# Performance work log

Measured on AMD Instinct MI355X. Metric: run time of the kernel, lower is better.

## Reference

```python
import jax, jax.numpy as jnp
import numpy as np

D_MODEL = 768
NUM_HEADS = 6
SPARSITY = 0.1
HEAD_DIM = D_MODEL // NUM_HEADS
SCALE = HEAD_DIM ** -0.5
B, C = 8, 4096


def setup_inputs() -> dict:
    key = jax.random.key(0)
    k1, k2 = jax.random.split(key, 2)
    x = jax.random.normal(k1, (B, C, D_MODEL), dtype=jnp.float32)
    # to_qkv: Linear(d_model, 3*d_model); torch layout W:[out,in], b:[out]
    W = jax.random.normal(k2, (3 * D_MODEL, D_MODEL), dtype=jnp.float32) * (D_MODEL ** -0.5)
    b = jnp.zeros((3 * D_MODEL,), dtype=jnp.float32)
    return {"x": x, "W": W, "b": b}


def reference(x, W, b):
    Bb, Cc, X = x.shape
    H, Dh = NUM_HEADS, HEAD_DIM
    n = Bb * Cc
    qkv = (x.reshape(n, X) @ W.T + b).reshape(n, 3, H, Dh)
    q, k, v = qkv[:, 0], qkv[:, 1], qkv[:, 2]  # each [n, H, Dh]
    # per-token attention across heads: [n, H, H]
    scores = jnp.einsum('nhd,ngd->nhg', q, k) * SCALE
    k_heads = max(1, int(H * SPARSITY))
    topk_scores, topk_idx = jax.lax.top_k(scores, k_heads)  # [n, H, k]
    soft = jax.nn.softmax(topk_scores, axis=-1)
    # sparse_attn @ v == weighted gather of v rows at topk_idx (zeros elsewhere)
    v_g = jnp.take_along_axis(v[:, None, :, :], topk_idx[..., None], axis=2)  # [n, H, k, Dh]
    out = jnp.einsum('nhk,nhkd->nhd', soft, v_g)  # [n, H, Dh]
    # torch: out.transpose(1, 2).reshape(B, C, d_model)  (3D tensor -> swap H and Dh)
    out = jnp.swapaxes(out, 1, 2).reshape(Bb, Cc, X)
    channel_importance = jnp.linalg.norm(out, axis=-1)  # [B, C]
    k_channels = max(1, int(Cc * SPARSITY))
    _, ch_idx = jax.lax.top_k(channel_importance, k_channels)  # [B, k_channels]
    sparse_feat = jnp.take_along_axis(out, ch_idx[:, :, None], axis=1)  # [B, k_channels, d_model]
    return sparse_feat, ch_idx, k_channels
```

## Files before the change

### kernel.cpp

```cpp
#include <hip/hip_runtime.h>
#include <cstdint>
#include <cstddef>

#pragma clang fp contract(off)

#define NROWS 32768
#define NCOLS 2304
#define DMODEL 768
#define QK 1536
#define KCH 409
#define NBATCH 8
#define FEAT_ELEMS ((size_t)NBATCH * KCH * DMODEL)
#define SCALE_F 0.08838834764831845f

#define BM 128
#define BN 128
#define BK 32
#define RS 140

__device__ __forceinline__ int chunk_off(int c) { return 8 * c + 4 * (c >> 2); }

__global__ __launch_bounds__(256) void gemm_qkv_f32(
    const float* __restrict__ x, const float* __restrict__ W,
    const float* __restrict__ bias, float* __restrict__ qkv)
{
    __shared__ float As[BK * RS];
    __shared__ float Bs[BK * RS];

    const int tid = threadIdx.x;
    const int tx = tid & 15;
    const int ty = tid >> 4;
    const int n0 = blockIdx.x * BN;
    const int m0 = blockIdx.y * BM;

    const int sm  = tid >> 3;
    const int sk4 = (tid & 7) << 2;

    const float* xa = x + (size_t)(m0 + sm) * DMODEL + sk4;
    const float* wb = W + (size_t)(n0 + sm) * DMODEL + sk4;

    const int aoff = chunk_off(ty);
    const int boff = chunk_off(tx);
    const int wsub = sm & 7;
    const int wchk = sm >> 3;

    float4 pa[4], pb[4];
    #pragma unroll
    for (int i = 0; i < 4; ++i) {
        pa[i] = *(const float4*)(xa + (size_t)(32 * i) * DMODEL);
        pb[i] = *(const float4*)(wb + (size_t)(32 * i) * DMODEL);
    }

    float acc[8][8] = {};

    for (int kt = 0; kt < DMODEL / BK; ++kt) {
        __syncthreads();
        #pragma unroll
        for (int i = 0; i < 4; ++i) {
            const int co = chunk_off(wchk + 4 * i) + wsub;
            As[(sk4 + 0) * RS + co] = pa[i].x;
            As[(sk4 + 1) * RS + co] = pa[i].y;
            As[(sk4 + 2) * RS + co] = pa[i].z;
            As[(sk4 + 3) * RS + co] = pa[i].w;
            Bs[(sk4 + 0) * RS + co] = pb[i].x;
            Bs[(sk4 + 1) * RS + co] = pb[i].y;
            Bs[(sk4 + 2) * RS + co] = pb[i].z;
            Bs[(sk4 + 3) * RS + co] = pb[i].w;
        }
        __syncthreads();

        if (kt + 1 < DMODEL / BK) {
            const int ko = (kt + 1) * BK;
            #pragma unroll
            for (int i = 0; i < 4; ++i) {
                pa[i] = *(const float4*)(xa + (size_t)(32 * i) * DMODEL + ko);
                pb[i] = *(const float4*)(wb + (size_t)(32 * i) * DMODEL + ko);
            }
        }

        #pragma unroll 8
        for (int k = 0; k < BK; ++k) {
            const float* ar = &As[k * RS + aoff];
            const float* br = &Bs[k * RS + boff];
            const float4 a0 = *(const float4*)(ar);
            const float4 a1 = *(const float4*)(ar + 4);
            const float4 b0 = *(const float4*)(br);
            const float4 b1 = *(const float4*)(br + 4);
            const float a[8] = {a0.x, a0.y, a0.z, a0.w, a1.x, a1.y, a1.z, a1.w};
            const float b[8] = {b0.x, b0.y, b0.z, b0.w, b1.x, b1.y, b1.z, b1.w};
            #pragma unroll
            for (int i = 0; i < 8; ++i)
                #pragma unroll
                for (int j = 0; j < 8; ++j)
                    acc[i][j] = fmaf(a[i], b[j], acc[i][j]);
        }
    }

    const int col = n0 + 8 * tx;
    float bcol[8];
    #pragma unroll
    for (int j = 0; j < 8; ++j) bcol[j] = bias[col + j];

    #pragma unroll
    for (int i = 0; i < 8; ++i) {
        const int row = m0 + 8 * ty + i;
        float4 o0, o1;
        o0.x = acc[i][0] + bcol[0];
        o0.y = acc[i][1] + bcol[1];
        o0.z = acc[i][2] + bcol[2];
        o0.w = acc[i][3] + bcol[3];
        o1.x = acc[i][4] + bcol[4];
        o1.y = acc[i][5] + bcol[5];
        o1.z = acc[i][6] + bcol[6];
        o1.w = acc[i][7] + bcol[7];
        *(float4*)(&qkv[(size_t)row * NCOLS + col])     = o0;
        *(float4*)(&qkv[(size_t)row * NCOLS + col + 4]) = o1;
    }
}

__global__ __launch_bounds__(256) void select_and_norm(
    const float* __restrict__ qkv, float* __restrict__ norms,
    uint64_t* __restrict__ gstar)
{
    __shared__ float rowbuf[4][NCOLS];
    __shared__ float sc[4][36];
    __shared__ int   gs_s[4][6];
    __shared__ float sblk[4][8];

    const int tid  = threadIdx.x;
    const int wave = tid >> 6;
    const int lane = tid & 63;
    const int n = blockIdx.x * 4 + wave;

    {
        const float4* src = (const float4*)(qkv + (size_t)n * NCOLS);
        float4* dst = (float4*)(&rowbuf[wave][0]);
        #pragma unroll
        for (int i = 0; i < 9; ++i) dst[lane + 64 * i] = src[lane + 64 * i];
    }
    __syncthreads();

    if (lane < 36) {
        const int h = lane / 6, g = lane % 6;
        const float* qh = &rowbuf[wave][h * 128];
        const float* kh = &rowbuf[wave][768 + g * 128];
        float s = 0.0f;
        for (int d = 0; d < 128; ++d)
            s = s + qh[d] * kh[d];
        sc[wave][lane] = s * SCALE_F;
    }
    __syncthreads();

    if (lane < 6) {
        float best = sc[wave][lane * 6];
        int bg = 0;
        #pragma unroll
        for (int g = 1; g < 6; ++g) {
            const float v = sc[wave][lane * 6 + g];
            if (v > best) { best = v; bg = g; }
        }
        gs_s[wave][lane] = bg;
    }
    __syncthreads();

    if (lane < 8) {
        const float* vr = &rowbuf[wave][QK];
        int gtab[6];
        #pragma unroll
        for (int h = 0; h < 6; ++h) gtab[h] = gs_s[wave][h];

        float r8[8];
        #pragma unroll
        for (int jj = 0; jj < 8; ++jj) {
            const int f = 96 * lane + jj;
            const float v = vr[gtab[f % 6] * 128 + f / 6];
            r8[jj] = v * v;
        }
        for (int i = 8; i < 96; i += 8) {
            #pragma unroll
            for (int jj = 0; jj < 8; ++jj) {
                const int f = 96 * lane + i + jj;
                const float v = vr[gtab[f % 6] * 128 + f / 6];
                r8[jj] = r8[jj] + v * v;
            }
        }
        sblk[wave][lane] = ((r8[0] + r8[1]) + (r8[2] + r8[3]))
                         + ((r8[4] + r8[5]) + (r8[6] + r8[7]));
    }
    __syncthreads();

    if (lane == 0) {
        const float* s = sblk[wave];
        float n2 = ((s[0] + s[1]) + (s[2] + s[3]))
                 + ((s[4] + s[5]) + (s[6] + s[7]));
        norms[n] = sqrtf(n2);
        uint64_t pk = 0;
        #pragma unroll
        for (int h = 0; h < 6; ++h)
            pk |= (uint64_t)gs_s[wave][h] << (8 * h);
        gstar[n] = pk;
    }
}

__global__ __launch_bounds__(256) void topk_channels(
    const float* __restrict__ norms, int* __restrict__ chidx,
    float* __restrict__ out)
{
    __shared__ float vals[4096];
    __shared__ float rv[256];
    __shared__ int   ri[256];
    const int b = blockIdx.x, t = threadIdx.x;

    for (int i = t; i < 4096; i += 256)
        vals[i] = norms[(size_t)b * 4096 + i];
    __syncthreads();

    for (int j = 0; j < KCH; ++j) {
        float best = -1.0f;
        int bi = 0;
        #pragma unroll
        for (int u = 0; u < 16; ++u) {
            const int i = t + 256 * u;
            const float v = vals[i];
            if (v > best) { best = v; bi = i; }
        }
        rv[t] = best; ri[t] = bi;
        __syncthreads();
        for (int s2 = 128; s2 > 0; s2 >>= 1) {
            if (t < s2) {
                const float ov = rv[t + s2]; const int oi = ri[t + s2];
                if (ov > rv[t] || (ov == rv[t] && oi < ri[t])) { rv[t] = ov; ri[t] = oi; }
            }
            __syncthreads();
        }
        if (t == 0) {
            const int w = ri[0];
            chidx[b * KCH + j] = w;
            out[FEAT_ELEMS + (size_t)b * KCH + j] = (float)w;
            vals[w] = -1.0f;
        }
        __syncthreads();
    }
    if (b == 0 && t == 0)
        out[FEAT_ELEMS + (size_t)NBATCH * KCH] = (float)KCH;
}

__global__ __launch_bounds__(256) void gather_sparse(
    const float* __restrict__ qkv, const uint64_t* __restrict__ gstar,
    const int* __restrict__ chidx, float* __restrict__ out)
{
    const int bj = blockIdx.x;
    const int b = bj / KCH;
    const int ch = chidx[bj];
    const int n = b * 4096 + ch;
    const uint64_t pk = gstar[n];
    for (int f = threadIdx.x; f < DMODEL; f += 256) {
        const int h = f % 6;
        const int d = f / 6;
        const int g = (int)((pk >> (8 * h)) & 7u);
        out[(size_t)bj * DMODEL + f] = qkv[(size_t)n * NCOLS + QK + g * 128 + d];
    }
}

extern "C" void kernel_launch(void* const* d_in, const int* in_sizes, int n_in,
                              void* d_out, int out_size, void* d_ws, size_t ws_size,
                              hipStream_t stream)
{
    const float* x    = (const float*)d_in[0];
    const float* W    = (const float*)d_in[1];
    const float* bias = (const float*)d_in[2];
    float* out = (float*)d_out;
    char*  ws  = (char*)d_ws;

    const size_t qkvBytes   = (size_t)NROWS * NCOLS * sizeof(float);
    const size_t normsBytes = (size_t)NROWS * sizeof(float);
    const size_t gstarBytes = (size_t)NROWS * sizeof(uint64_t);
    const size_t chidxBytes = (size_t)NBATCH * KCH * sizeof(int);
    const size_t baseBytes  = qkvBytes + normsBytes + gstarBytes + chidxBytes;
    if (ws_size < baseBytes) return;

    float*    qkv   = (float*)ws;
    float*    norms = (float*)(ws + qkvBytes);
    uint64_t* gstar = (uint64_t*)(ws + qkvBytes + normsBytes);
    int*      chidx = (int*)(ws + qkvBytes + normsBytes + gstarBytes);

    gemm_qkv_f32<<<dim3(NCOLS / BN, NROWS / BM), 256, 0, stream>>>(x, W, bias, qkv);
    select_and_norm<<<NROWS / 4, 256, 0, stream>>>(qkv, norms, gstar);
    topk_channels<<<NBATCH, 256, 0, stream>>>(norms, chidx, out);
    gather_sparse<<<NBATCH * KCH, 256, 0, stream>>>(qkv, gstar, chidx, out);
}
```

Measured before the change: 1.996 ms.

## Enlarge QKV GEMM tile to 256x128 with XOR-swizzled shared memory layout

Doubles the M tile of the fp32 QKV GEMM so each thread computes a 16x8 accumulator block, raising FMA work per shared-memory load. The shared-memory chunk placement is XOR-permuted by k-group to avoid bank conflicts, with separate row strides for the A and B tiles. Launch bounds now request two blocks per CU. The 128 accumulators plus prefetch registers raise register pressure and could cause spills or lower occupancy.

```diff
diff --git a/kernel.cpp b/kernel.cpp
--- a/kernel.cpp
+++ b/kernel.cpp
@@ -13,19 +13,20 @@
 #define FEAT_ELEMS ((size_t)NBATCH * KCH * DMODEL)
 #define SCALE_F 0.08838834764831845f
 
-#define BM 128
+#define BM 256
 #define BN 128
 #define BK 32
-#define RS 140
+#define RSA 284
+#define RSB 140
 
 __device__ __forceinline__ int chunk_off(int c) { return 8 * c + 4 * (c >> 2); }
 
-__global__ __launch_bounds__(256) void gemm_qkv_f32(
+__global__ __launch_bounds__(256, 2) void gemm_qkv_f32(
     const float* __restrict__ x, const float* __restrict__ W,
     const float* __restrict__ bias, float* __restrict__ qkv)
 {
-    __shared__ float As[BK * RS];
-    __shared__ float Bs[BK * RS];
+    __shared__ float As[BK * RSA];
+    __shared__ float Bs[BK * RSB];
 
     const int tid = threadIdx.x;
     const int tx = tid & 15;
@@ -35,64 +36,78 @@
 
     const int sm  = tid >> 3;
     const int sk4 = (tid & 7) << 2;
+    const int perm_s = (sk4 >> 2) & 7;
+    const int wsub = sm & 7;
+    const int wchk = sm >> 3;
 
     const float* xa = x + (size_t)(m0 + sm) * DMODEL + sk4;
     const float* wb = W + (size_t)(n0 + sm) * DMODEL + sk4;
 
-    const int aoff = chunk_off(ty);
-    const int boff = chunk_off(tx);
-    const int wsub = sm & 7;
-    const int wchk = sm >> 3;
-
-    float4 pa[4], pb[4];
-    #pragma unroll
-    for (int i = 0; i < 4; ++i) {
-        pa[i] = *(const float4*)(xa + (size_t)(32 * i) * DMODEL);
-        pb[i] = *(const float4*)(wb + (size_t)(32 * i) * DMODEL);
-    }
-
-    float acc[8][8] = {};
+    int coa[8], cob[4];
+    #pragma unroll
+    for (int i = 0; i < 8; ++i) coa[i] = chunk_off((wchk + 4 * i) ^ perm_s) + wsub;
+    #pragma unroll
+    for (int i = 0; i < 4; ++i) cob[i] = chunk_off((wchk + 4 * i) ^ perm_s) + wsub;
+
+    float4 pa[8], pb[4];
+    #pragma unroll
+    for (int i = 0; i < 8; ++i) pa[i] = *(const float4*)(xa + (size_t)(32 * i) * DMODEL);
+    #pragma unroll
+    for (int i = 0; i < 4; ++i) pb[i] = *(const float4*)(wb + (size_t)(32 * i) * DMODEL);
+
+    float acc[16][8] = {};
 
     for (int kt = 0; kt < DMODEL / BK; ++kt) {
         __syncthreads();
         #pragma unroll
+        for (int i = 0; i < 8; ++i) {
+            As[(sk4 + 0) * RSA + coa[i]] = pa[i].x;
+            As[(sk4 + 1) * RSA + coa[i]] = pa[i].y;
+            As[(sk4 + 2) * RSA + coa[i]] = pa[i].z;
+            As[(sk4 + 3) * RSA + coa[i]] = pa[i].w;
+        }
+        #pragma unroll
         for (int i = 0; i < 4; ++i) {
-            const int co = chunk_off(wchk + 4 * i) + wsub;
-            As[(sk4 + 0) * RS + co] = pa[i].x;
-            As[(sk4 + 1) * RS + co] = pa[i].y;
-            As[(sk4 + 2) * RS + co] = pa[i].z;
-            As[(sk4 + 3) * RS + co] = pa[i].w;
-            Bs[(sk4 + 0) * RS + co] = pb[i].x;
-            Bs[(sk4 + 1) * RS + co] = pb[i].y;
-            Bs[(sk4 + 2) * RS + co] = pb[i].z;
-            Bs[(sk4 + 3) * RS + co] = pb[i].w;
+            Bs[(sk4 + 0) * RSB + cob[i]] = pb[i].x;
+            Bs[(sk4 + 1) * RSB + cob[i]] = pb[i].y;
+            Bs[(sk4 + 2) * RSB + cob[i]] = pb[i].z;
+            Bs[(sk4 + 3) * RSB + cob[i]] = pb[i].w;
         }
         __syncthreads();
 
         if (kt + 1 < DMODEL / BK) {
             const int ko = (kt + 1) * BK;
             #pragma unroll
-            for (int i = 0; i < 4; ++i) {
+            for (int i = 0; i < 8; ++i)
                 pa[i] = *(const float4*)(xa + (size_t)(32 * i) * DMODEL + ko);
+            #pragma unroll
+            for (int i = 0; i < 4; ++i)
                 pb[i] = *(const float4*)(wb + (size_t)(32 * i) * DMODEL + ko);
+        }
+
+        #pragma unroll
+        for (int p = 0; p < 8; ++p) {
+            const float* Ap0 = &As[chunk_off((2 * ty) ^ p)];
+            const float* Ap1 = &As[chunk_off((2 * ty + 1) ^ p)];
+            const float* Bp  = &Bs[chunk_off(tx ^ p)];
+            #pragma unroll
+            for (int kq = 0; kq < 4; ++kq) {
+                const int k = 4 * p + kq;
+                const float4 a0 = *(const float4*)(Ap0 + k * RSA);
+                const float4 a1 = *(const float4*)(Ap0 + k * RSA + 4);
+                const float4 a2 = *(const float4*)(Ap1 + k * RSA);
+                const float4 a3 = *(const float4*)(Ap1 + k * RSA + 4);
+                const float4 b0 = *(const float4*)(Bp + k * RSB);
+                const float4 b1 = *(const float4*)(Bp + k * RSB + 4);
+                const float a[16] = {a0.x, a0.y, a0.z, a0.w, a1.x, a1.y, a1.z, a1.w,
+                                     a2.x, a2.y, a2.z, a2.w, a3.x, a3.y, a3.z, a3.w};
+                const float b[8]  = {b0.x, b0.y, b0.z, b0.w, b1.x, b1.y, b1.z, b1.w};
+                #pragma unroll
+                for (int i = 0; i < 16; ++i)
+                    #pragma unroll
+                    for (int j = 0; j < 8; ++j)
+                        acc[i][j] = fmaf(a[i], b[j], acc[i][j]);
             }
-        }
-
-        #pragma unroll 8
-        for (int k = 0; k < BK; ++k) {
-            const float* ar = &As[k * RS + aoff];
-            const float* br = &Bs[k * RS + boff];
-            const float4 a0 = *(const float4*)(ar);
-            const float4 a1 = *(const float4*)(ar + 4);
-            const float4 b0 = *(const float4*)(br);
-            const float4 b1 = *(const float4*)(br + 4);
-            const float a[8] = {a0.x, a0.y, a0.z, a0.w, a1.x, a1.y, a1.z, a1.w};
-            const float b[8] = {b0.x, b0.y, b0.z, b0.w, b1.x, b1.y, b1.z, b1.w};
-            #pragma unroll
-            for (int i = 0; i < 8; ++i)
-                #pragma unroll
-                for (int j = 0; j < 8; ++j)
-                    acc[i][j] = fmaf(a[i], b[j], acc[i][j]);
         }
     }
 
@@ -102,8 +117,8 @@
     for (int j = 0; j < 8; ++j) bcol[j] = bias[col + j];
 
     #pragma unroll
-    for (int i = 0; i < 8; ++i) {
-        const int row = m0 + 8 * ty + i;
+    for (int i = 0; i < 16; ++i) {
+        const int row = m0 + 16 * ty + i;
         float4 o0, o1;
         o0.x = acc[i][0] + bcol[0];
         o0.y = acc[i][1] + bcol[1];
```

Measured after the change: 4.147 ms. 2.08x slower.
